# Kernel optimization log

Hardware: AMD Instinct MI355X
Metric: run time of the kernel (lower is better)

Reference implementation:

```python
import jax, jax.numpy as jnp
import numpy as np

NUM_HEADS = 4
NUM_GROUPS = 32
EPS = 1e-5


def setup_inputs() -> dict:
    key = jax.random.key(0)
    ks = jax.random.split(key, 4)
    ch = 256
    x = jax.random.normal(ks[0], (16, ch, 32, 32), dtype=jnp.float32)
    gn_w = jnp.ones((ch,), jnp.float32)
    gn_b = jnp.zeros((ch,), jnp.float32)
    # conv1x1 weights, kaiming-ish scale
    qkv_w = jax.random.normal(ks[1], (3 * ch, ch), dtype=jnp.float32) / np.sqrt(ch)
    qkv_b = jnp.zeros((3 * ch,), jnp.float32)
    proj_w = jax.random.normal(ks[2], (ch, ch), dtype=jnp.float32) / np.sqrt(ch)
    proj_b = jnp.zeros((ch,), jnp.float32)
    return {"x": x, "gn_w": gn_w, "gn_b": gn_b, "qkv_w": qkv_w,
            "qkv_b": qkv_b, "proj_w": proj_w, "proj_b": proj_b}


def _group_norm(x, w, b):
    bsz, c, h, wd = x.shape
    g = NUM_GROUPS
    xg = x.reshape(bsz, g, c // g, h, wd)
    mean = xg.mean(axis=(2, 3, 4), keepdims=True)
    var = xg.var(axis=(2, 3, 4), keepdims=True)
    xg = (xg - mean) * jax.lax.rsqrt(var + EPS)
    return xg.reshape(bsz, c, h, wd) * w[None, :, None, None] + b[None, :, None, None]


def reference(x, gn_w, gn_b, qkv_w, qkv_b, proj_w, proj_b):
    b, c, h, w = x.shape
    hd = c // NUM_HEADS
    scale = hd ** (-0.5)
    y = _group_norm(x, gn_w, gn_b)
    # 1x1 conv == channel matmul
    qkv = jnp.einsum('oc,bchw->bohw', qkv_w, y) + qkv_b[None, :, None, None]
    q, k, v = jnp.split(qkv, 3, axis=1)
    q = q.reshape(b, NUM_HEADS, hd, h * w)
    k = k.reshape(b, NUM_HEADS, hd, h * w)
    v = v.reshape(b, NUM_HEADS, hd, h * w)
    attn = jnp.einsum('bhdi,bhdj->bhij', q * scale, k)
    attn = jax.nn.softmax(attn, axis=-1)
    out = jnp.einsum('bhij,bhdj->bhdi', attn, v)
    out = out.reshape(b, c, h, w)
    out = jnp.einsum('oc,bchw->bohw', proj_w, out) + proj_b[None, :, None, None]
    return x + out
```

## Files before the change

### kernel.cpp

```cpp
#include <hip/hip_runtime.h>
#include <cstddef>

#define B_   16
#define C_   256
#define HW_  1024
#define NH_  4
#define NG_  32
#define CPG_ 8
#define CS_  0.18033688f

typedef __attribute__((ext_vector_type(8))) short bf16x8;
typedef __attribute__((ext_vector_type(8))) _Float16 f16x8;
typedef __attribute__((ext_vector_type(4))) float f32x4;

#define MFMA16B(a, b, c) __builtin_amdgcn_mfma_f32_16x16x32_bf16(a, b, c, 0, 0, 0)
#define MFMA16H(a, b, c) __builtin_amdgcn_mfma_f32_16x16x32_f16(a, b, c, 0, 0, 0)

__device__ __forceinline__ float bf2f(unsigned short h) {
    unsigned int u = ((unsigned int)h) << 16;
    return __builtin_bit_cast(float, u);
}
__device__ __forceinline__ unsigned short f2bf(float f) {
    unsigned int u = __builtin_bit_cast(unsigned int, f);
    u += 0x7FFFu + ((u >> 16) & 1u);
    return (unsigned short)(u >> 16);
}
__device__ __forceinline__ unsigned packbf(float a, float b) {
    unsigned ua = __builtin_bit_cast(unsigned, a) + 0x8000u;
    unsigned ub = __builtin_bit_cast(unsigned, b) + 0x8000u;
    return __builtin_amdgcn_perm(ub, ua, 0x07060302u);
}
__device__ __forceinline__ unsigned pkh(float a, float b) {
    auto h2 = __builtin_amdgcn_cvt_pkrtz(a, b);
    return __builtin_bit_cast(unsigned, h2);
}

__global__ __launch_bounds__(256) void wcvt_kernel(
    const float* __restrict__ qw, const float* __restrict__ pw,
    unsigned short* __restrict__ oq, unsigned short* __restrict__ op)
{
    int i = blockIdx.x * 256 + threadIdx.x;
    const float* s; unsigned short* d; int j;
    if (i < 49152) { s = qw; d = oq; j = i; }
    else           { s = pw; d = op; j = i - 49152; }
    float4 f = ((const float4*)s)[j];
    uint2 u = {pkh(f.x, f.y), pkh(f.z, f.w)};
    *(uint2*)&d[(size_t)j * 4] = u;
}

__global__ __launch_bounds__(256) void gn_kernel(
    const float* __restrict__ x,
    const float* __restrict__ gw,
    const float* __restrict__ gb,
    float2* __restrict__ scsh)
{
    int blk = blockIdx.x;
    const float* xg = x + (size_t)blk * CPG_ * HW_;
    const int N = CPG_ * HW_;

    float s = 0.f, ss = 0.f;
    for (int e = threadIdx.x * 4; e < N; e += 1024) {
        float4 v4 = *(const float4*)&xg[e];
        s  += v4.x + v4.y + v4.z + v4.w;
        ss += v4.x * v4.x + v4.y * v4.y + v4.z * v4.z + v4.w * v4.w;
    }
    #pragma unroll
    for (int off = 32; off > 0; off >>= 1) {
        s  += __shfl_down(s, off, 64);
        ss += __shfl_down(ss, off, 64);
    }
    __shared__ float red[8];
    __shared__ float2 stf;
    int lane = threadIdx.x & 63, wv = threadIdx.x >> 6;
    if (lane == 0) { red[wv] = s; red[4 + wv] = ss; }
    __syncthreads();
    if (threadIdx.x == 0) {
        float S  = red[0] + red[1] + red[2] + red[3];
        float SS = red[4] + red[5] + red[6] + red[7];
        float mean = S / (float)N;
        float var  = SS / (float)N - mean * mean;
        stf = make_float2(mean, rsqrtf(var + 1e-5f));
    }
    __syncthreads();
    if (threadIdx.x < 8) {
        int ch = (blk & 31) * CPG_ + threadIdx.x;
        float sc = stf.y * gw[ch];
        float sh = gb[ch] - stf.x * sc;
        scsh[blk * 8 + threadIdx.x] = make_float2(sc, sh);
    }
}

template <bool FUSE_GN, bool FINAL>
__global__ __launch_bounds__(256) void gemm_mfma_kernel(
    const unsigned short* __restrict__ W16,
    const float* __restrict__ Xf,
    const unsigned short* __restrict__ Xh,
    const float* __restrict__ bias,
    const float2* __restrict__ scsh,
    const float* __restrict__ res,
    float* __restrict__ outF,
    unsigned short* __restrict__ qT,
    unsigned short* __restrict__ kT,
    unsigned short* __restrict__ vN,
    int M, int K, int N)
{
    __shared__ union {
        struct { unsigned short A[2][128][40]; unsigned short Bt[2][64][40]; } st;
        unsigned short nd[2][64][72];
        unsigned short mn[128][72];
    } L;

    const int b  = blockIdx.z;
    const int m0 = blockIdx.y * 128, n0 = blockIdx.x * 64;
    const int t  = threadIdx.x;
    const int l15 = t & 15, quad = (t >> 4) & 3;
    const int wave = t >> 6, wm = wave >> 1, wn = wave & 1;

    union HF { uint4 q; f16x8 v; };

    f32x4 acc[4][2];
    #pragma unroll
    for (int mt = 0; mt < 4; ++mt)
        #pragma unroll
        for (int nt = 0; nt < 2; ++nt)
            acc[mt][nt] = (f32x4){0.f, 0.f, 0.f, 0.f};

    const int ar = t >> 1, akh = (t & 1) * 16;
    const int bn = t & 63, bkb = t >> 6;

    uint4 pa0, pa1;
    float pv[8];
    unsigned short ph[8];
    float2 ss[8];

    auto PREF = [&](int k0) {
        const unsigned short* wp = &W16[(size_t)(m0 + ar) * K + k0 + akh];
        pa0 = *(const uint4*)wp;
        pa1 = *(const uint4*)(wp + 8);
        int ch = k0 + bkb * 8;
        if (FINAL) {
            const unsigned short* xp = &Xh[((size_t)b * K + ch) * N + n0 + bn];
            #pragma unroll
            for (int j = 0; j < 8; ++j) ph[j] = xp[(size_t)j * N];
        } else {
            const float* xp = &Xf[((size_t)b * K + ch) * N + n0 + bn];
            #pragma unroll
            for (int j = 0; j < 8; ++j) pv[j] = xp[(size_t)j * N];
            if (FUSE_GN) {
                const float4* sp = (const float4*)&scsh[b * C_ + ch];
                #pragma unroll
                for (int q2 = 0; q2 < 4; ++q2) ((float4*)ss)[q2] = sp[q2];
            }
        }
    };

    PREF(0);
    const int NIT = K / 32;
    for (int it = 0; it < NIT; ++it) {
        const int bsel = it & 1;
        *(uint4*)&L.st.A[bsel][ar][akh]     = pa0;
        *(uint4*)&L.st.A[bsel][ar][akh + 8] = pa1;
        {
            float v[8];
            if (FINAL) {
                #pragma unroll
                for (int j = 0; j < 8; ++j) v[j] = bf2f(ph[j]);
            } else {
                #pragma unroll
                for (int j = 0; j < 8; ++j) v[j] = pv[j];
                if (FUSE_GN) {
                    #pragma unroll
                    for (int j = 0; j < 8; ++j) v[j] = v[j] * ss[j].x + ss[j].y;
                }
            }
            uint4 bw = {pkh(v[0], v[1]), pkh(v[2], v[3]), pkh(v[4], v[5]), pkh(v[6], v[7])};
            *(uint4*)&L.st.Bt[bsel][bn][bkb * 8] = bw;
        }
        __syncthreads();
        if (it + 1 < NIT) PREF((it + 1) * 32);
        HF af[4], bfv[2];
        #pragma unroll
        for (int mt = 0; mt < 4; ++mt)
            af[mt].q = *(const uint4*)&L.st.A[bsel][wm * 64 + mt * 16 + l15][quad * 8];
        #pragma unroll
        for (int nt = 0; nt < 2; ++nt)
            bfv[nt].q = *(const uint4*)&L.st.Bt[bsel][wn * 32 + nt * 16 + l15][quad * 8];
        #pragma unroll
        for (int mt = 0; mt < 4; ++mt)
            #pragma unroll
            for (int nt = 0; nt < 2; ++nt)
                acc[mt][nt] = MFMA16H(af[mt].v, bfv[nt].v, acc[mt][nt]);
    }
    __syncthreads();

    if (FINAL) {
        #pragma unroll
        for (int mt = 0; mt < 4; ++mt) {
            #pragma unroll
            for (int rr = 0; rr < 4; ++rr) {
                int m = m0 + wm * 64 + mt * 16 + quad * 4 + rr;
                float bv = bias[m];
                #pragma unroll
                for (int nt = 0; nt < 2; ++nt) {
                    int n = n0 + wn * 32 + nt * 16 + l15;
                    size_t off = ((size_t)b * M + m) * (size_t)N + n;
                    outF[off] = acc[mt][nt][rr] + bv + res[off];
                }
            }
        }
    } else if (m0 < 512) {
        const float qsc = (m0 < 256) ? CS_ : 1.f;
        #pragma unroll
        for (int mt = 0; mt < 4; ++mt)
            #pragma unroll
            for (int rr = 0; rr < 4; ++rr) {
                int dl = mt * 16 + quad * 4 + rr;
                float bv = bias[m0 + wm * 64 + dl];
                #pragma unroll
                for (int nt = 0; nt < 2; ++nt)
                    L.nd[wm][wn * 32 + nt * 16 + l15][dl] = f2bf((acc[mt][nt][rr] + bv) * qsc);
            }
        __syncthreads();
        unsigned short* dst = (m0 < 256) ? qT : kT;
        int headbase = (m0 & 255) >> 6;
        int hl = t >> 7, tt = t & 127;
        int nl = tt >> 1, db = (tt & 1) * 32;
        const unsigned short* src = &L.nd[hl][nl][db];
        unsigned short* gp = &dst[(((size_t)(b * 4 + headbase + hl)) * 1024 + n0 + nl) * 64 + db];
        uint4 u0 = *(const uint4*)(src);
        uint4 u1 = *(const uint4*)(src + 8);
        uint4 u2 = *(const uint4*)(src + 16);
        uint4 u3 = *(const uint4*)(src + 24);
        *(uint4*)(gp)      = u0;
        *(uint4*)(gp + 8)  = u1;
        *(uint4*)(gp + 16) = u2;
        *(uint4*)(gp + 24) = u3;
    } else {
        #pragma unroll
        for (int mt = 0; mt < 4; ++mt)
            #pragma unroll
            for (int rr = 0; rr < 4; ++rr) {
                int ml = wm * 64 + mt * 16 + quad * 4 + rr;
                float bv = bias[m0 + ml];
                #pragma unroll
                for (int nt = 0; nt < 2; ++nt)
                    L.mn[ml][wn * 32 + nt * 16 + l15] = f2bf(acc[mt][nt][rr] + bv);
            }
        __syncthreads();
        int ml = t & 127, nb = t >> 7;
        const unsigned short* src = &L.mn[ml][nb * 32];
        unsigned short* gp = &vN[((size_t)b * 256 + (m0 - 512) + ml) * 1024 + n0 + nb * 32];
        uint4 u0 = *(const uint4*)(src);
        uint4 u1 = *(const uint4*)(src + 8);
        uint4 u2 = *(const uint4*)(src + 16);
        uint4 u3 = *(const uint4*)(src + 24);
        *(uint4*)(gp)      = u0;
        *(uint4*)(gp + 8)  = u1;
        *(uint4*)(gp + 16) = u2;
        *(uint4*)(gp + 24) = u3;
    }
}

__global__ __launch_bounds__(256) void attn_mfma_kernel(
    const unsigned short* __restrict__ qT,
    const unsigned short* __restrict__ kT,
    const unsigned short* __restrict__ vN,
    unsigned short* __restrict__ OP,
    float* __restrict__ LP)
{
    __shared__ unsigned short Kt[2][64][72];
    __shared__ unsigned short Vs[2][64][72];

    const int t    = threadIdx.x;
    const int wv   = t >> 6;
    const int l15  = t & 15;
    const int quad = (t >> 4) & 3;
    const int bh   = blockIdx.x;
    const int i0   = blockIdx.y * 128;
    const int jh   = blockIdx.z;

    union FragU { uint4 q; unsigned u[4]; bf16x8 v; };

    FragU qf[2][2];
    {
        const unsigned short* qg = qT + (size_t)bh * (1024 * 64);
        int qrow = i0 + wv * 32 + l15;
        #pragma unroll
        for (int nt = 0; nt < 2; ++nt)
            #pragma unroll
            for (int kt = 0; kt < 2; ++kt)
                qf[nt][kt].q = *(const uint4*)&qg[(size_t)(qrow + nt * 16) * 64 + kt * 32 + quad * 8];
    }

    f32x4 accO[4][2];
    #pragma unroll
    for (int m = 0; m < 4; ++m)
        #pragma unroll
        for (int n = 0; n < 2; ++n)
            accO[m][n] = (f32x4){0.f, 0.f, 0.f, 0.f};
    float l_i[2] = {0.f, 0.f};

    const unsigned short* kg = kT + (size_t)bh * (1024 * 64);
    const unsigned short* vg = vN + (size_t)bh * (64 * 1024);

    const int slbase = l15 + ((quad & 1) << 5);
    const bool upper = (t & 32) != 0;
    const int sr = t >> 2, sc = (t & 3) * 16;

    uint4 kr0, kr1, vr0, vr1;
    {
        const int j0 = jh * 512;
        const unsigned short* kp = &kg[(size_t)(j0 + sr) * 64 + sc];
        const unsigned short* vp = &vg[(size_t)sr * 1024 + j0 + sc];
        kr0 = *(const uint4*)kp;  kr1 = *(const uint4*)(kp + 8);
        vr0 = *(const uint4*)vp;  vr1 = *(const uint4*)(vp + 8);
    }

    for (int it = 0; it < 8; ++it) {
        const int bsel = it & 1;
        *(uint4*)&Kt[bsel][sr][sc]     = kr0;
        *(uint4*)&Kt[bsel][sr][sc + 8] = kr1;
        *(uint4*)&Vs[bsel][sr][sc]     = vr0;
        *(uint4*)&Vs[bsel][sr][sc + 8] = vr1;
        __syncthreads();
        if (it < 7) {
            const int j0n = jh * 512 + (it + 1) * 64;
            const unsigned short* kp = &kg[(size_t)(j0n + sr) * 64 + sc];
            const unsigned short* vp = &vg[(size_t)sr * 1024 + j0n + sc];
            kr0 = *(const uint4*)kp;  kr1 = *(const uint4*)(kp + 8);
            vr0 = *(const uint4*)vp;  vr1 = *(const uint4*)(vp + 8);
        }

        f32x4 accS[4][2];
        #pragma unroll
        for (int mt = 0; mt < 4; ++mt) {
            FragU ak[2];
            #pragma unroll
            for (int kt = 0; kt < 2; ++kt)
                ak[kt].q = *(const uint4*)&Kt[bsel][mt * 16 + l15][kt * 32 + quad * 8];
            #pragma unroll
            for (int nt = 0; nt < 2; ++nt) {
                f32x4 z = (f32x4){0.f, 0.f, 0.f, 0.f};
                z = MFMA16B(ak[0].v, qf[nt][0].v, z);
                z = MFMA16B(ak[1].v, qf[nt][1].v, z);
                accS[mt][nt] = z;
            }
        }

        float rs[2] = {0.f, 0.f};
        unsigned pk[4][2][2];
        #pragma unroll
        for (int mt = 0; mt < 4; ++mt)
            #pragma unroll
            for (int nt = 0; nt < 2; ++nt) {
                float p0 = exp2f(accS[mt][nt][0]);
                float p1 = exp2f(accS[mt][nt][1]);
                float p2 = exp2f(accS[mt][nt][2]);
                float p3 = exp2f(accS[mt][nt][3]);
                rs[nt] += (p0 + p1) + (p2 + p3);
                pk[mt][nt][0] = packbf(p0, p1);
                pk[mt][nt][1] = packbf(p2, p3);
            }
        #pragma unroll
        for (int nt = 0; nt < 2; ++nt) {
            float r = rs[nt];
            r += __shfl_xor(r, 16, 64);
            r += __shfl_xor(r, 32, 64);
            l_i[nt] += r;
        }

        FragU bfr[2][2];
        #pragma unroll
        for (int kt = 0; kt < 2; ++kt)
            #pragma unroll
            for (int nt = 0; nt < 2; ++nt)
                #pragma unroll
                for (int w4 = 0; w4 < 4; ++w4) {
                    int sl = slbase + ((w4 >> 1) << 4);
                    int lo = __shfl((int)pk[2 * kt + 0][nt][w4 & 1], sl, 64);
                    int hi = __shfl((int)pk[2 * kt + 1][nt][w4 & 1], sl, 64);
                    bfr[kt][nt].u[w4] = (unsigned)(upper ? hi : lo);
                }

        #pragma unroll
        for (int mtd = 0; mtd < 4; ++mtd) {
            FragU av[2];
            #pragma unroll
            for (int kt = 0; kt < 2; ++kt)
                av[kt].q = *(const uint4*)&Vs[bsel][mtd * 16 + l15][kt * 32 + quad * 8];
            #pragma unroll
            for (int nt = 0; nt < 2; ++nt) {
                accO[mtd][nt] = MFMA16B(av[0].v, bfr[0][nt].v, accO[mtd][nt]);
                accO[mtd][nt] = MFMA16B(av[1].v, bfr[1][nt].v, accO[mtd][nt]);
            }
        }
    }

    unsigned short* ob = OP + ((size_t)jh * 64 + bh) * (64 * 1024) + i0 + wv * 32;
    #pragma unroll
    for (int mtd = 0; mtd < 4; ++mtd)
        #pragma unroll
        for (int nt = 0; nt < 2; ++nt)
            #pragma unroll
            for (int rr = 0; rr < 4; ++rr) {
                int d = mtd * 16 + quad * 4 + rr;
                ob[(size_t)d * 1024 + nt * 16 + l15] = f2bf(accO[mtd][nt][rr]);
            }
    if (quad == 0) {
        float* lp = &LP[((size_t)jh * 64 + bh) * 1024 + i0 + wv * 32 + l15];
        lp[0]  = l_i[0];
        lp[16] = l_i[1];
    }
}

__global__ __launch_bounds__(256) void attn_combine_kernel(
    const unsigned short* __restrict__ OP,
    const float* __restrict__ LP,
    unsigned short* __restrict__ att)
{
    size_t e0 = ((size_t)blockIdx.x * 256 + threadIdx.x) * 4;
    int bh  = (int)(e0 >> 16);
    int col = (int)(e0 & 1023);
    ushort4 a = *(const ushort4*)&OP[e0];
    ushort4 b = *(const ushort4*)&OP[(size_t)(1 << 22) + e0];
    float4 la = *(const float4*)&LP[(size_t)bh * 1024 + col];
    float4 lb = *(const float4*)&LP[(size_t)(1 << 16) + (size_t)bh * 1024 + col];
    ushort4 o;
    o.x = f2bf((bf2f(a.x) + bf2f(b.x)) / (la.x + lb.x));
    o.y = f2bf((bf2f(a.y) + bf2f(b.y)) / (la.y + lb.y));
    o.z = f2bf((bf2f(a.z) + bf2f(b.z)) / (la.z + lb.z));
    o.w = f2bf((bf2f(a.w) + bf2f(b.w)) / (la.w + lb.w));
    *(ushort4*)&att[e0] = o;
}

extern "C" void kernel_launch(void* const* d_in, const int* in_sizes, int n_in,
                              void* d_out, int out_size, void* d_ws, size_t ws_size,
                              hipStream_t stream)
{
    const float* x      = (const float*)d_in[0];
    const float* gn_w   = (const float*)d_in[1];
    const float* gn_b   = (const float*)d_in[2];
    const float* qkv_w  = (const float*)d_in[3];
    const float* qkv_b  = (const float*)d_in[4];
    const float* proj_w = (const float*)d_in[5];
    const float* proj_b = (const float*)d_in[6];
    float* out = (float*)d_out;

    char* ws = (char*)d_ws;
    float2* scsh = (float2*)ws;
    unsigned short* w16q = (unsigned short*)(ws + 32768);
    unsigned short* w16p = w16q + 768 * 256;
    unsigned short* qT   = w16p + 256 * 256;
    unsigned short* kT   = qT + (size_t)B_ * NH_ * HW_ * 64;
    unsigned short* vN   = kT + (size_t)B_ * NH_ * HW_ * 64;
    unsigned short* att  = vN + (size_t)B_ * C_ * HW_;
    unsigned short* OP   = att + (size_t)B_ * C_ * HW_;
    float*          LP   = (float*)(OP + (size_t)2 * B_ * C_ * HW_);
    (void)in_sizes; (void)n_in; (void)out_size; (void)ws_size;

    wcvt_kernel<<<dim3(256), 256, 0, stream>>>(qkv_w, proj_w, w16q, w16p);
    gn_kernel<<<dim3(B_ * NG_), 256, 0, stream>>>(x, gn_w, gn_b, scsh);

    gemm_mfma_kernel<true, false><<<dim3(HW_ / 64, (3 * C_) / 128, B_), 256, 0, stream>>>(
        w16q, x, nullptr, qkv_b, scsh, nullptr, nullptr,
        qT, kT, vN, 3 * C_, C_, HW_);

    attn_mfma_kernel<<<dim3(NH_ * B_, HW_ / 128, 2), 256, 0, stream>>>(qT, kT, vN, OP, LP);
    attn_combine_kernel<<<dim3(4096), 256, 0, stream>>>(OP, LP, att);

    gemm_mfma_kernel<false, true><<<dim3(HW_ / 64, C_ / 128, B_), 256, 0, stream>>>(
        w16p, nullptr, att, proj_b, nullptr, x, out,
        nullptr, nullptr, nullptr, C_, C_, HW_);
}
```

Before: 160.6 us.

## Fuse split-attention combine into projection GEMM and use K=16 MFMA for PV

```diff
diff --git a/kernel.cpp b/kernel.cpp
--- a/kernel.cpp
+++ b/kernel.cpp
@@ -10,11 +10,19 @@
 #define CS_  0.18033688f
 
 typedef __attribute__((ext_vector_type(8))) short bf16x8;
+typedef __attribute__((ext_vector_type(4))) short s16x4;
 typedef __attribute__((ext_vector_type(8))) _Float16 f16x8;
 typedef __attribute__((ext_vector_type(4))) float f32x4;
 
 #define MFMA16B(a, b, c) __builtin_amdgcn_mfma_f32_16x16x32_bf16(a, b, c, 0, 0, 0)
 #define MFMA16H(a, b, c) __builtin_amdgcn_mfma_f32_16x16x32_f16(a, b, c, 0, 0, 0)
+
+#if __has_builtin(__builtin_amdgcn_mfma_f32_16x16x16bf16_1k)
+#define HAVE_MFMA16K16 1
+#define MFMA16B4(a, b, c) __builtin_amdgcn_mfma_f32_16x16x16bf16_1k(a, b, c, 0, 0, 0)
+#else
+#define HAVE_MFMA16K16 0
+#endif
 
 __device__ __forceinline__ float bf2f(unsigned short h) {
     unsigned int u = ((unsigned int)h) << 16;
@@ -94,7 +102,8 @@
 __global__ __launch_bounds__(256) void gemm_mfma_kernel(
     const unsigned short* __restrict__ W16,
     const float* __restrict__ Xf,
-    const unsigned short* __restrict__ Xh,
+    const unsigned short* __restrict__ OP,
+    const float* __restrict__ LPp,
     const float* __restrict__ bias,
     const float2* __restrict__ scsh,
     const float* __restrict__ res,
@@ -128,9 +137,21 @@
     const int ar = t >> 1, akh = (t & 1) * 16;
     const int bn = t & 63, bkb = t >> 6;
 
+    float rinv[4];
+    if (FINAL) {
+        int n = n0 + bn;
+        #pragma unroll
+        for (int h = 0; h < 4; ++h) {
+            float l0 = LPp[(size_t)(b * 4 + h) * 1024 + n];
+            float l1 = LPp[(size_t)(64 + b * 4 + h) * 1024 + n];
+            rinv[h] = 1.f / (l0 + l1);
+        }
+    }
+
     uint4 pa0, pa1;
     float pv[8];
-    unsigned short ph[8];
+    unsigned short ph0[8], ph1[8];
+    int   pH = 0;
     float2 ss[8];
 
     auto PREF = [&](int k0) {
@@ -139,9 +160,13 @@
         pa1 = *(const uint4*)(wp + 8);
         int ch = k0 + bkb * 8;
         if (FINAL) {
-            const unsigned short* xp = &Xh[((size_t)b * K + ch) * N + n0 + bn];
-            #pragma unroll
-            for (int j = 0; j < 8; ++j) ph[j] = xp[(size_t)j * N];
+            pH = ch >> 6;
+            size_t base = ((size_t)(b * 4 + pH) * 64 + (ch & 63)) * 1024 + n0 + bn;
+            #pragma unroll
+            for (int j = 0; j < 8; ++j) {
+                ph0[j] = OP[base + (size_t)j * 1024];
+                ph1[j] = OP[(size_t)64 * 64 * 1024 + base + (size_t)j * 1024];
+            }
         } else {
             const float* xp = &Xf[((size_t)b * K + ch) * N + n0 + bn];
             #pragma unroll
@@ -163,8 +188,10 @@
         {
             float v[8];
             if (FINAL) {
-                #pragma unroll
-                for (int j = 0; j < 8; ++j) v[j] = bf2f(ph[j]);
+                float ri = rinv[pH];
+                #pragma unroll
+                for (int j = 0; j < 8; ++j)
+                    v[j] = (bf2f(ph0[j]) + bf2f(ph1[j])) * ri;
             } else {
                 #pragma unroll
                 for (int j = 0; j < 8; ++j) v[j] = pv[j];
@@ -299,12 +326,17 @@
         for (int n = 0; n < 2; ++n)
             accO[m][n] = (f32x4){0.f, 0.f, 0.f, 0.f};
     float l_i[2] = {0.f, 0.f};
+#if HAVE_MFMA16K16
+    f32x4 accL[2] = {(f32x4){0.f, 0.f, 0.f, 0.f}, (f32x4){0.f, 0.f, 0.f, 0.f}};
+    const s16x4 ones4 = {(short)0x3F80, (short)0x3F80, (short)0x3F80, (short)0x3F80};
+#endif
 
     const unsigned short* kg = kT + (size_t)bh * (1024 * 64);
     const unsigned short* vg = vN + (size_t)bh * (64 * 1024);
 
     const int slbase = l15 + ((quad & 1) << 5);
     const bool upper = (t & 32) != 0;
+    (void)slbase; (void)upper;
     const int sr = t >> 2, sc = (t & 3) * 16;
 
     uint4 kr0, kr1, vr0, vr1;
@@ -347,6 +379,38 @@
             }
         }
 
+#if HAVE_MFMA16K16
+        union PB { unsigned u[2]; s16x4 v; };
+        PB pb[4][2];
+        #pragma unroll
+        for (int mt = 0; mt < 4; ++mt)
+            #pragma unroll
+            for (int nt = 0; nt < 2; ++nt) {
+                float p0 = exp2f(accS[mt][nt][0]);
+                float p1 = exp2f(accS[mt][nt][1]);
+                float p2 = exp2f(accS[mt][nt][2]);
+                float p3 = exp2f(accS[mt][nt][3]);
+                pb[mt][nt].u[0] = packbf(p0, p1);
+                pb[mt][nt].u[1] = packbf(p2, p3);
+            }
+        #pragma unroll
+        for (int mt = 0; mt < 4; ++mt)
+            #pragma unroll
+            for (int nt = 0; nt < 2; ++nt)
+                accL[nt] = MFMA16B4(ones4, pb[mt][nt].v, accL[nt]);
+        #pragma unroll
+        for (int mtd = 0; mtd < 4; ++mtd) {
+            union AV { uint2 d; s16x4 v; } av[4];
+            #pragma unroll
+            for (int mt = 0; mt < 4; ++mt)
+                av[mt].d = *(const uint2*)&Vs[bsel][mtd * 16 + l15][mt * 16 + quad * 4];
+            #pragma unroll
+            for (int nt = 0; nt < 2; ++nt)
+                #pragma unroll
+                for (int mt = 0; mt < 4; ++mt)
+                    accO[mtd][nt] = MFMA16B4(av[mt].v, pb[mt][nt].v, accO[mtd][nt]);
+        }
+#else
         float rs[2] = {0.f, 0.f};
         unsigned pk[4][2][2];
         #pragma unroll
@@ -368,7 +432,6 @@
             r += __shfl_xor(r, 32, 64);
             l_i[nt] += r;
         }
-
         FragU bfr[2][2];
         #pragma unroll
         for (int kt = 0; kt < 2; ++kt)
@@ -381,7 +444,6 @@
                     int hi = __shfl((int)pk[2 * kt + 1][nt][w4 & 1], sl, 64);
                     bfr[kt][nt].u[w4] = (unsigned)(upper ? hi : lo);
                 }
-
         #pragma unroll
         for (int mtd = 0; mtd < 4; ++mtd) {
             FragU av[2];
@@ -394,7 +456,13 @@
                 accO[mtd][nt] = MFMA16B(av[1].v, bfr[1][nt].v, accO[mtd][nt]);
             }
         }
-    }
+#endif
+    }
+
+#if HAVE_MFMA16K16
+    l_i[0] = accL[0][0];
+    l_i[1] = accL[1][0];
+#endif
 
     unsigned short* ob = OP + ((size_t)jh * 64 + bh) * (64 * 1024) + i0 + wv * 32;
     #pragma unroll
@@ -411,26 +479,6 @@
         lp[0]  = l_i[0];
         lp[16] = l_i[1];
     }
-}
-
-__global__ __launch_bounds__(256) void attn_combine_kernel(
-    const unsigned short* __restrict__ OP,
-    const float* __restrict__ LP,
-    unsigned short* __restrict__ att)
-{
-    size_t e0 = ((size_t)blockIdx.x * 256 + threadIdx.x) * 4;
-    int bh  = (int)(e0 >> 16);
-    int col = (int)(e0 & 1023);
-    ushort4 a = *(const ushort4*)&OP[e0];
-    ushort4 b = *(const ushort4*)&OP[(size_t)(1 << 22) + e0];
-    float4 la = *(const float4*)&LP[(size_t)bh * 1024 + col];
-    float4 lb = *(const float4*)&LP[(size_t)(1 << 16) + (size_t)bh * 1024 + col];
-    ushort4 o;
-    o.x = f2bf((bf2f(a.x) + bf2f(b.x)) / (la.x + lb.x));
-    o.y = f2bf((bf2f(a.y) + bf2f(b.y)) / (la.y + lb.y));
-    o.z = f2bf((bf2f(a.z) + bf2f(b.z)) / (la.z + lb.z));
-    o.w = f2bf((bf2f(a.w) + bf2f(b.w)) / (la.w + lb.w));
-    *(ushort4*)&att[e0] = o;
 }
 
 extern "C" void kernel_launch(void* const* d_in, const int* in_sizes, int n_in,
@@ -453,8 +501,7 @@
     unsigned short* qT   = w16p + 256 * 256;
     unsigned short* kT   = qT + (size_t)B_ * NH_ * HW_ * 64;
     unsigned short* vN   = kT + (size_t)B_ * NH_ * HW_ * 64;
-    unsigned short* att  = vN + (size_t)B_ * C_ * HW_;
-    unsigned short* OP   = att + (size_t)B_ * C_ * HW_;
+    unsigned short* OP   = vN + (size_t)B_ * C_ * HW_;
     float*          LP   = (float*)(OP + (size_t)2 * B_ * C_ * HW_);
     (void)in_sizes; (void)n_in; (void)out_size; (void)ws_size;
 
@@ -462,13 +509,12 @@
     gn_kernel<<<dim3(B_ * NG_), 256, 0, stream>>>(x, gn_w, gn_b, scsh);
 
     gemm_mfma_kernel<true, false><<<dim3(HW_ / 64, (3 * C_) / 128, B_), 256, 0, stream>>>(
-        w16q, x, nullptr, qkv_b, scsh, nullptr, nullptr,
+        w16q, x, nullptr, nullptr, qkv_b, scsh, nullptr, nullptr,
         qT, kT, vN, 3 * C_, C_, HW_);
 
     attn_mfma_kernel<<<dim3(NH_ * B_, HW_ / 128, 2), 256, 0, stream>>>(qT, kT, vN, OP, LP);
-    attn_combine_kernel<<<dim3(4096), 256, 0, stream>>>(OP, LP, att);
 
     gemm_mfma_kernel<false, true><<<dim3(HW_ / 64, C_ / 128, B_), 256, 0, stream>>>(
-        w16p, nullptr, att, proj_b, nullptr, x, out,
+        w16p, nullptr, OP, LP, proj_b, nullptr, x, out,
         nullptr, nullptr, nullptr, C_, C_, HW_);
 }
```

Measured after the change: 149.7 us. 6.8% less time.
